# Optimization experiments

Measured on AMD Instinct MI355X. Metric: run time of the kernel, lower is better.

Reference implementation:

```python
import jax, jax.numpy as jnp
import numpy as np


def toeplitz_from(weight_matrix):
    # Faithful to the torch Toeplitz parametrization:
    # parameters = concat(W[::-1, 0], W[0, 1:]); toep[i, j] = parameters[n_rows-1-i+j]
    n_rows, n_cols = weight_matrix.shape
    params = jnp.concatenate([weight_matrix[::-1, 0], weight_matrix[0, 1:]])
    idx = (n_rows - 1) - jnp.arange(n_rows)[:, None] + jnp.arange(n_cols)[None, :]
    return params[idx]  # [n_rows, n_cols], built in one gather instead of a loop


def setup_inputs() -> dict:
    key = jax.random.key(0)
    ks = jax.random.split(key, 8)
    B, frame_dim, esn_dim, last_dim = 65536, 64, 960, 1024
    comb = frame_dim + esn_dim
    s1 = 1.0 / np.sqrt(comb)
    s2 = 1.0 / np.sqrt(last_dim)
    return {
        "x_frame": jax.random.normal(ks[0], (B, frame_dim), jnp.float32),
        "h_esn": jax.random.normal(ks[1], (B, esn_dim), jnp.float32),
        "W1": jax.random.normal(ks[2], (last_dim, comb), jnp.float32) * s1,
        "b1": jax.random.normal(ks[3], (last_dim,), jnp.float32) * s1,
        "W_slope": jax.random.normal(ks[4], (frame_dim, last_dim), jnp.float32) * s2,
        "b_slope": jax.random.normal(ks[5], (frame_dim,), jnp.float32) * s2,
        "W_int": jax.random.normal(ks[6], (frame_dim, last_dim), jnp.float32) * s2,
        "b_int": jax.random.normal(ks[7], (frame_dim,), jnp.float32) * s2,
    }


def reference(x_frame, h_esn, W1, b1, W_slope, b_slope, W_int, b_int):
    W1_toep = toeplitz_from(W1)                      # [last_dim, frame+esn]
    combined = jnp.concatenate([x_frame, h_esn], axis=-1)  # [B, frame+esn]
    q_last = jax.nn.relu(combined @ W1_toep.T + b1)  # [B, last_dim]
    slope = jnp.tanh(q_last @ W_slope.T + b_slope)   # [B, frame_dim]
    intercept = q_last @ W_int.T + b_int             # [B, frame_dim]
    return slope, intercept
```

## Files before the change

kernel.cpp:

```cpp
#include <hip/hip_runtime.h>
#include <cstdint>
#include <cstddef>

typedef __bf16 bf16x8v __attribute__((ext_vector_type(8)));
typedef float f32x4v __attribute__((ext_vector_type(4)));

__device__ __forceinline__ void gload_lds16(const void* g, void* l) {
  __builtin_amdgcn_global_load_lds((const __attribute__((address_space(1))) void*)g,
                                   (__attribute__((address_space(3))) void*)l,
                                   16, 0, 0);
}

__device__ __forceinline__ bf16x8v cvt_bf16x8(f32x4v a, f32x4v b) {
  bf16x8v r;
  r[0] = (__bf16)a[0]; r[1] = (__bf16)a[1]; r[2] = (__bf16)a[2]; r[3] = (__bf16)a[3];
  r[4] = (__bf16)b[0]; r[5] = (__bf16)b[1]; r[6] = (__bf16)b[2]; r[7] = (__bf16)b[3];
  return r;
}

__global__ __launch_bounds__(256) void prep_kernel(const float* __restrict__ W1,
                                                   const float* __restrict__ Wslope,
                                                   const float* __restrict__ Wint,
                                                   __bf16* __restrict__ toep,
                                                   __bf16* __restrict__ Wcat) {
  int id = blockIdx.x * 256 + threadIdx.x;
  if (id < 1024 * 1024) {
    int i = id >> 10, j = id & 1023;
    int p = 1023 - i + j;
    float v = (p < 1024) ? W1[(size_t)(1023 - p) << 10]
                         : W1[p - 1023];
    toep[id] = (__bf16)v;
  } else {
    int id2 = id - 1024 * 1024;
    int n = id2 >> 10, k = id2 & 1023;
    float v = (n < 64) ? Wslope[((size_t)n << 10) + k] : Wint[((size_t)(n - 64) << 10) + k];
    Wcat[id2] = (__bf16)v;
  }
}

__global__ __launch_bounds__(256) void gemm1_kernel(const float* __restrict__ x,
                                                    const float* __restrict__ h,
                                                    const __bf16* __restrict__ toep,
                                                    const float* __restrict__ b1,
                                                    __bf16* __restrict__ q) {
  __shared__ __align__(16) __bf16 At[128 * 32];
  __shared__ __align__(16) __bf16 Bt[128 * 32];
  const int tid = threadIdx.x;
  const int wid = tid >> 6;
  const int lane = tid & 63;
  const int wrow = wid >> 1, wcol = wid & 1;
  const int m0 = (blockIdx.x >> 3) << 7;
  const int n0 = (blockIdx.x & 7) << 7;
  const int quad = lane >> 4, l15 = lane & 15;
  const int rl = lane >> 2, seg = lane & 3;

  f32x4v acc[4][4] = {};

  auto a_ptr = [&](int k0, int t) -> const f32x4v* {
    const float* s; int ld, kk;
    if (k0 < 64) { s = x; ld = 64; kk = k0; } else { s = h; ld = 960; kk = k0 - 64; }
    int row = m0 + wid * 32 + t * 16 + rl;
    return (const f32x4v*)(s + (size_t)row * ld + kk + seg * 8);
  };

  f32x4v pv[2][2];
  {
    const f32x4v* p0 = a_ptr(0, 0); pv[0][0] = p0[0]; pv[0][1] = p0[1];
    const f32x4v* p1 = a_ptr(0, 1); pv[1][0] = p1[0]; pv[1][1] = p1[1];
  }

  for (int k0 = 0; k0 < 1024; k0 += 32) {
    __syncthreads();
    {
      int rb = wid * 32;
#pragma unroll
      for (int c = 0; c < 2; ++c) {
        int row = rb + c * 16 + rl;
        const __bf16* g = toep + (((size_t)(n0 + row)) << 10) + k0 + seg * 8;
        gload_lds16(g, &Bt[(rb + c * 16) * 32]);
      }
    }
#pragma unroll
    for (int t = 0; t < 2; ++t) {
      int row = wid * 32 + t * 16 + rl;
      *(bf16x8v*)&At[row * 32 + seg * 8] = cvt_bf16x8(pv[t][0], pv[t][1]);
    }
    __syncthreads();
    if (k0 + 32 < 1024) {
      const f32x4v* p0 = a_ptr(k0 + 32, 0);
      f32x4v n00 = p0[0], n01 = p0[1];
      const f32x4v* p1 = a_ptr(k0 + 32, 1);
      f32x4v n10 = p1[0], n11 = p1[1];
      pv[0][0] = n00; pv[0][1] = n01; pv[1][0] = n10; pv[1][1] = n11;
    }
    bf16x8v af[4], bfr[4];
#pragma unroll
    for (int r = 0; r < 4; ++r)
      af[r] = *(const bf16x8v*)&At[(wrow * 64 + r * 16 + l15) * 32 + quad * 8];
#pragma unroll
    for (int c = 0; c < 4; ++c)
      bfr[c] = *(const bf16x8v*)&Bt[(wcol * 64 + c * 16 + l15) * 32 + quad * 8];
#pragma unroll
    for (int r = 0; r < 4; ++r)
#pragma unroll
      for (int c = 0; c < 4; ++c)
        acc[r][c] = __builtin_amdgcn_mfma_f32_16x16x32_bf16(af[r], bfr[c], acc[r][c], 0, 0, 0);
  }

#pragma unroll
  for (int c = 0; c < 4; ++c) {
    int col = n0 + wcol * 64 + c * 16 + l15;
    float bias = b1[col];
#pragma unroll
    for (int r = 0; r < 4; ++r)
#pragma unroll
      for (int e = 0; e < 4; ++e) {
        int row = m0 + wrow * 64 + r * 16 + quad * 4 + e;
        float v = fmaxf(acc[r][c][e] + bias, 0.0f);
        q[((size_t)row << 10) + col] = (__bf16)v;
      }
  }
}

__global__ __launch_bounds__(256) void gemm2_kernel(const __bf16* __restrict__ q,
                                                    const __bf16* __restrict__ Wcat,
                                                    const float* __restrict__ b_slope,
                                                    const float* __restrict__ b_int,
                                                    float* __restrict__ out) {
  __shared__ __align__(16) __bf16 At[128 * 32];
  __shared__ __align__(16) __bf16 Bt[128 * 32];
  const int tid = threadIdx.x;
  const int wid = tid >> 6, lane = tid & 63;
  const int wrow = wid >> 1, wcol = wid & 1;
  const int m0 = blockIdx.x << 7;
  const int quad = lane >> 4, l15 = lane & 15;
  const int rl = lane >> 2, seg = lane & 3;

  f32x4v acc[4][4] = {};

  for (int k0 = 0; k0 < 1024; k0 += 32) {
    __syncthreads();
#pragma unroll
    for (int c = 0; c < 2; ++c) {
      int row = wid * 32 + c * 16 + rl;
      gload_lds16(q + (((size_t)(m0 + row)) << 10) + k0 + seg * 8, &At[(wid * 32 + c * 16) * 32]);
      gload_lds16(Wcat + (((size_t)row) << 10) + k0 + seg * 8, &Bt[(wid * 32 + c * 16) * 32]);
    }
    __syncthreads();
    bf16x8v af[4], bfr[4];
#pragma unroll
    for (int r = 0; r < 4; ++r)
      af[r] = *(const bf16x8v*)&At[(wrow * 64 + r * 16 + l15) * 32 + quad * 8];
#pragma unroll
    for (int c = 0; c < 4; ++c)
      bfr[c] = *(const bf16x8v*)&Bt[(wcol * 64 + c * 16 + l15) * 32 + quad * 8];
#pragma unroll
    for (int r = 0; r < 4; ++r)
#pragma unroll
      for (int c = 0; c < 4; ++c)
        acc[r][c] = __builtin_amdgcn_mfma_f32_16x16x32_bf16(af[r], bfr[c], acc[r][c], 0, 0, 0);
  }

#pragma unroll
  for (int c = 0; c < 4; ++c) {
    int col = wcol * 64 + c * 16 + l15;
    float bias = (col < 64) ? b_slope[col] : b_int[col - 64];
#pragma unroll
    for (int r = 0; r < 4; ++r)
#pragma unroll
      for (int e = 0; e < 4; ++e) {
        int row = m0 + wrow * 64 + r * 16 + quad * 4 + e;
        float v = acc[r][c][e] + bias;
        if (col < 64) {
          float xc = fminf(fmaxf(v, -15.f), 15.f);
          float t = __expf(2.f * xc);
          out[(size_t)row * 64 + col] = (t - 1.f) / (t + 1.f);
        } else {
          out[(size_t)4194304 + (size_t)row * 64 + (col - 64)] = v;
        }
      }
  }
}

extern "C" void kernel_launch(void* const* d_in, const int* in_sizes, int n_in,
                              void* d_out, int out_size, void* d_ws, size_t ws_size,
                              hipStream_t stream) {
  const float* x  = (const float*)d_in[0];
  const float* h  = (const float*)d_in[1];
  const float* W1 = (const float*)d_in[2];
  const float* b1 = (const float*)d_in[3];
  const float* Ws = (const float*)d_in[4];
  const float* bs = (const float*)d_in[5];
  const float* Wi = (const float*)d_in[6];
  const float* bi = (const float*)d_in[7];
  char* ws = (char*)d_ws;
  __bf16* q    = (__bf16*)ws;
  __bf16* toep = (__bf16*)(ws + (size_t)134217728);
  __bf16* Wcat = (__bf16*)(ws + (size_t)134217728 + (size_t)2097152);

  hipLaunchKernelGGL(prep_kernel,  dim3(4608), dim3(256), 0, stream, W1, Ws, Wi, toep, Wcat);
  hipLaunchKernelGGL(gemm1_kernel, dim3(4096), dim3(256), 0, stream, x, h, toep, b1, q);
  hipLaunchKernelGGL(gemm2_kernel, dim3(512),  dim3(256), 0, stream, q, Wcat, bs, bi, (float*)d_out);
}
```

Baseline: 648.7 us.

## Pre-pack inputs to bf16 and double-buffer both GEMMs with direct LDS loads

A separate pack kernel converts x/h into one concatenated bf16 activation matrix and builds the Toeplitz and output weights with vectorized writes from a small params vector. GEMM1 then loads both operands via global_load_lds into double-buffered LDS with one barrier per k-step, so register conversion and the second barrier leave the main loop. GEMM2 uses 64-row tiles with a k-step of 64 and double buffering, doubling its grid. The cost is an extra 128MB bf16 write and read of the activations plus a larger workspace, with a fallback to the old path when the workspace is too small.

```diff
diff --git a/kernel.cpp b/kernel.cpp
--- a/kernel.cpp
+++ b/kernel.cpp
@@ -16,6 +16,247 @@
   r[0] = (__bf16)a[0]; r[1] = (__bf16)a[1]; r[2] = (__bf16)a[2]; r[3] = (__bf16)a[3];
   r[4] = (__bf16)b[0]; r[5] = (__bf16)b[1]; r[6] = (__bf16)b[2]; r[7] = (__bf16)b[3];
   return r;
+}
+
+__global__ __launch_bounds__(256) void params_kernel(const float* __restrict__ W1,
+                                                     float* __restrict__ params) {
+  int p = blockIdx.x * 256 + threadIdx.x;
+  if (p < 2047)
+    params[p] = (p < 1024) ? W1[(size_t)(1023 - p) << 10] : W1[p - 1023];
+}
+
+__global__ __launch_bounds__(256) void pack_kernel(const float* __restrict__ x,
+                                                   const float* __restrict__ h,
+                                                   const float* __restrict__ params,
+                                                   const float* __restrict__ Ws,
+                                                   const float* __restrict__ Wi,
+                                                   __bf16* __restrict__ Acat,
+                                                   __bf16* __restrict__ toep,
+                                                   __bf16* __restrict__ Wcat) {
+  long u = (long)blockIdx.x * 256 + threadIdx.x;
+  if (u < 8388608L) {
+    int r = (int)(u >> 7), cg = (int)(u & 127);
+    const float* s = (cg < 8) ? x + (size_t)r * 64 + cg * 8
+                              : h + (size_t)r * 960 + (cg - 8) * 8;
+    f32x4v a = *(const f32x4v*)s, b = *(const f32x4v*)(s + 4);
+    *(bf16x8v*)(Acat + ((size_t)r << 10) + cg * 8) = cvt_bf16x8(a, b);
+  } else if (u < 8519680L) {
+    long t = u - 8388608L;
+    int i = (int)(t >> 7), j0 = (int)(t & 127) * 8;
+    const float* s = params + (1023 - i + j0);
+    bf16x8v o;
+#pragma unroll
+    for (int e = 0; e < 8; ++e) o[e] = (__bf16)s[e];
+    *(bf16x8v*)(toep + ((size_t)i << 10) + j0) = o;
+  } else {
+    long t = u - 8519680L;
+    int n = (int)(t >> 7), k0 = (int)(t & 127) * 8;
+    const float* s = (n < 64) ? Ws + ((size_t)n << 10) + k0
+                              : Wi + ((size_t)(n - 64) << 10) + k0;
+    f32x4v a = *(const f32x4v*)s, b = *(const f32x4v*)(s + 4);
+    *(bf16x8v*)(Wcat + ((size_t)n << 10) + k0) = cvt_bf16x8(a, b);
+  }
+}
+
+__global__ __launch_bounds__(256) void gemm1_dma(const __bf16* __restrict__ Acat,
+                                                 const __bf16* __restrict__ toep,
+                                                 const float* __restrict__ b1,
+                                                 __bf16* __restrict__ q) {
+  __shared__ __align__(16) __bf16 Ab[2][128 * 32];
+  __shared__ __align__(16) __bf16 Bb[2][128 * 32];
+  const int tid = threadIdx.x, wid = tid >> 6, lane = tid & 63;
+  const int wrow = wid >> 1, wcol = wid & 1;
+  const int m0 = (blockIdx.x >> 3) << 7;
+  const int n0 = (blockIdx.x & 7) << 7;
+  const int quad = lane >> 4, l15 = lane & 15;
+  const int rl = lane >> 2, seg = lane & 3;
+
+  f32x4v acc[4][4] = {};
+
+  auto stage = [&](int buf, int kt) {
+    int k0 = kt << 5;
+#pragma unroll
+    for (int c = 0; c < 2; ++c) {
+      int rb = wid * 32 + c * 16;
+      gload_lds16(Acat + (((size_t)(m0 + rb + rl)) << 10) + k0 + seg * 8, &Ab[buf][rb * 32]);
+      gload_lds16(toep + (((size_t)(n0 + rb + rl)) << 10) + k0 + seg * 8, &Bb[buf][rb * 32]);
+    }
+  };
+
+  stage(0, 0);
+  for (int kt = 0; kt < 32; ++kt) {
+    int cur = kt & 1;
+    __syncthreads();
+    if (kt < 31) stage(cur ^ 1, kt + 1);
+    bf16x8v af[4], bfr[4];
+#pragma unroll
+    for (int r = 0; r < 4; ++r)
+      af[r] = *(const bf16x8v*)&Ab[cur][(wrow * 64 + r * 16 + l15) * 32 + quad * 8];
+#pragma unroll
+    for (int c = 0; c < 4; ++c)
+      bfr[c] = *(const bf16x8v*)&Bb[cur][(wcol * 64 + c * 16 + l15) * 32 + quad * 8];
+#pragma unroll
+    for (int r = 0; r < 4; ++r)
+#pragma unroll
+      for (int c = 0; c < 4; ++c)
+        acc[r][c] = __builtin_amdgcn_mfma_f32_16x16x32_bf16(af[r], bfr[c], acc[r][c], 0, 0, 0);
+  }
+
+#pragma unroll
+  for (int c = 0; c < 4; ++c) {
+    int col = n0 + wcol * 64 + c * 16 + l15;
+    float bias = b1[col];
+#pragma unroll
+    for (int r = 0; r < 4; ++r)
+#pragma unroll
+      for (int e = 0; e < 4; ++e) {
+        int row = m0 + wrow * 64 + r * 16 + quad * 4 + e;
+        q[((size_t)row << 10) + col] = (__bf16)fmaxf(acc[r][c][e] + bias, 0.0f);
+      }
+  }
+}
+
+__global__ __launch_bounds__(256) void gemm1_fused(const float* __restrict__ x,
+                                                   const float* __restrict__ h,
+                                                   const __bf16* __restrict__ toep,
+                                                   const float* __restrict__ b1,
+                                                   __bf16* __restrict__ q) {
+  __shared__ __align__(16) __bf16 At[128 * 32];
+  __shared__ __align__(16) __bf16 Bt[128 * 32];
+  const int tid = threadIdx.x, wid = tid >> 6, lane = tid & 63;
+  const int wrow = wid >> 1, wcol = wid & 1;
+  const int m0 = (blockIdx.x >> 3) << 7;
+  const int n0 = (blockIdx.x & 7) << 7;
+  const int quad = lane >> 4, l15 = lane & 15;
+  const int rl = lane >> 2, seg = lane & 3;
+
+  f32x4v acc[4][4] = {};
+  auto a_ptr = [&](int k0, int t) -> const f32x4v* {
+    const float* s; int ld, kk;
+    if (k0 < 64) { s = x; ld = 64; kk = k0; } else { s = h; ld = 960; kk = k0 - 64; }
+    int row = m0 + wid * 32 + t * 16 + rl;
+    return (const f32x4v*)(s + (size_t)row * ld + kk + seg * 8);
+  };
+  f32x4v pv[2][2];
+  { const f32x4v* p0 = a_ptr(0, 0); pv[0][0] = p0[0]; pv[0][1] = p0[1];
+    const f32x4v* p1 = a_ptr(0, 1); pv[1][0] = p1[0]; pv[1][1] = p1[1]; }
+
+  for (int k0 = 0; k0 < 1024; k0 += 32) {
+    __syncthreads();
+    { int rb = wid * 32;
+#pragma unroll
+      for (int c = 0; c < 2; ++c) {
+        int row = rb + c * 16 + rl;
+        gload_lds16(toep + (((size_t)(n0 + row)) << 10) + k0 + seg * 8, &Bt[(rb + c * 16) * 32]);
+      } }
+#pragma unroll
+    for (int t = 0; t < 2; ++t) {
+      int row = wid * 32 + t * 16 + rl;
+      *(bf16x8v*)&At[row * 32 + seg * 8] = cvt_bf16x8(pv[t][0], pv[t][1]);
+    }
+    __syncthreads();
+    if (k0 + 32 < 1024) {
+      const f32x4v* p0 = a_ptr(k0 + 32, 0); f32x4v n00 = p0[0], n01 = p0[1];
+      const f32x4v* p1 = a_ptr(k0 + 32, 1); f32x4v n10 = p1[0], n11 = p1[1];
+      pv[0][0] = n00; pv[0][1] = n01; pv[1][0] = n10; pv[1][1] = n11;
+    }
+    bf16x8v af[4], bfr[4];
+#pragma unroll
+    for (int r = 0; r < 4; ++r)
+      af[r] = *(const bf16x8v*)&At[(wrow * 64 + r * 16 + l15) * 32 + quad * 8];
+#pragma unroll
+    for (int c = 0; c < 4; ++c)
+      bfr[c] = *(const bf16x8v*)&Bt[(wcol * 64 + c * 16 + l15) * 32 + quad * 8];
+#pragma unroll
+    for (int r = 0; r < 4; ++r)
+#pragma unroll
+      for (int c = 0; c < 4; ++c)
+        acc[r][c] = __builtin_amdgcn_mfma_f32_16x16x32_bf16(af[r], bfr[c], acc[r][c], 0, 0, 0);
+  }
+#pragma unroll
+  for (int c = 0; c < 4; ++c) {
+    int col = n0 + wcol * 64 + c * 16 + l15;
+    float bias = b1[col];
+#pragma unroll
+    for (int r = 0; r < 4; ++r)
+#pragma unroll
+      for (int e = 0; e < 4; ++e) {
+        int row = m0 + wrow * 64 + r * 16 + quad * 4 + e;
+        q[((size_t)row << 10) + col] = (__bf16)fmaxf(acc[r][c][e] + bias, 0.0f);
+      }
+  }
+}
+
+__global__ __launch_bounds__(256) void gemm2_dma(const __bf16* __restrict__ q,
+                                                 const __bf16* __restrict__ Wcat,
+                                                 const float* __restrict__ b_slope,
+                                                 const float* __restrict__ b_int,
+                                                 float* __restrict__ out) {
+  __shared__ __align__(16) __bf16 Ab[2][64 * 64];
+  __shared__ __align__(16) __bf16 Bb[2][128 * 64];
+  const int tid = threadIdx.x, wid = tid >> 6, lane = tid & 63;
+  const int wrow = wid >> 1, wcol = wid & 1;
+  const int m0 = blockIdx.x << 6;
+  const int quad = lane >> 4, l15 = lane & 15;
+  const int r8 = lane >> 3, s8 = lane & 7;
+
+  f32x4v acc[2][4] = {};
+
+  auto stage = [&](int buf, int kt) {
+    int k0 = kt << 6;
+#pragma unroll
+    for (int j = 0; j < 2; ++j) {
+      int rb = wid * 16 + j * 8;
+      gload_lds16(q + (((size_t)(m0 + rb + r8)) << 10) + k0 + s8 * 8, &Ab[buf][rb * 64]);
+    }
+#pragma unroll
+    for (int j = 0; j < 4; ++j) {
+      int rb = wid * 32 + j * 8;
+      gload_lds16(Wcat + (((size_t)(rb + r8)) << 10) + k0 + s8 * 8, &Bb[buf][rb * 64]);
+    }
+  };
+
+  stage(0, 0);
+  for (int kt = 0; kt < 16; ++kt) {
+    int cur = kt & 1;
+    __syncthreads();
+    if (kt < 15) stage(cur ^ 1, kt + 1);
+#pragma unroll
+    for (int s = 0; s < 2; ++s) {
+      bf16x8v af[2], bfr[4];
+#pragma unroll
+      for (int r = 0; r < 2; ++r)
+        af[r] = *(const bf16x8v*)&Ab[cur][(wrow * 32 + r * 16 + l15) * 64 + s * 32 + quad * 8];
+#pragma unroll
+      for (int c = 0; c < 4; ++c)
+        bfr[c] = *(const bf16x8v*)&Bb[cur][(wcol * 64 + c * 16 + l15) * 64 + s * 32 + quad * 8];
+#pragma unroll
+      for (int r = 0; r < 2; ++r)
+#pragma unroll
+        for (int c = 0; c < 4; ++c)
+          acc[r][c] = __builtin_amdgcn_mfma_f32_16x16x32_bf16(af[r], bfr[c], acc[r][c], 0, 0, 0);
+    }
+  }
+
+#pragma unroll
+  for (int c = 0; c < 4; ++c) {
+    int col = wcol * 64 + c * 16 + l15;
+    float bias = (col < 64) ? b_slope[col] : b_int[col - 64];
+#pragma unroll
+    for (int r = 0; r < 2; ++r)
+#pragma unroll
+      for (int e = 0; e < 4; ++e) {
+        int row = m0 + wrow * 32 + r * 16 + quad * 4 + e;
+        float v = acc[r][c][e] + bias;
+        if (col < 64) {
+          float xc = fminf(fmaxf(v, -15.f), 15.f);
+          float t = __expf(2.f * xc);
+          out[(size_t)row * 64 + col] = (t - 1.f) / (t + 1.f);
+        } else {
+          out[(size_t)4194304 + (size_t)row * 64 + (col - 64)] = v;
+        }
+      }
+  }
 }
 
 __global__ __launch_bounds__(256) void prep_kernel(const float* __restrict__ W1,
@@ -27,158 +268,13 @@
   if (id < 1024 * 1024) {
     int i = id >> 10, j = id & 1023;
     int p = 1023 - i + j;
-    float v = (p < 1024) ? W1[(size_t)(1023 - p) << 10]
-                         : W1[p - 1023];
+    float v = (p < 1024) ? W1[(size_t)(1023 - p) << 10] : W1[p - 1023];
     toep[id] = (__bf16)v;
   } else {
     int id2 = id - 1024 * 1024;
     int n = id2 >> 10, k = id2 & 1023;
     float v = (n < 64) ? Wslope[((size_t)n << 10) + k] : Wint[((size_t)(n - 64) << 10) + k];
     Wcat[id2] = (__bf16)v;
-  }
-}
-
-__global__ __launch_bounds__(256) void gemm1_kernel(const float* __restrict__ x,
-                                                    const float* __restrict__ h,
-                                                    const __bf16* __restrict__ toep,
-                                                    const float* __restrict__ b1,
-                                                    __bf16* __restrict__ q) {
-  __shared__ __align__(16) __bf16 At[128 * 32];
-  __shared__ __align__(16) __bf16 Bt[128 * 32];
-  const int tid = threadIdx.x;
-  const int wid = tid >> 6;
-  const int lane = tid & 63;
-  const int wrow = wid >> 1, wcol = wid & 1;
-  const int m0 = (blockIdx.x >> 3) << 7;
-  const int n0 = (blockIdx.x & 7) << 7;
-  const int quad = lane >> 4, l15 = lane & 15;
-  const int rl = lane >> 2, seg = lane & 3;
-
-  f32x4v acc[4][4] = {};
-
-  auto a_ptr = [&](int k0, int t) -> const f32x4v* {
-    const float* s; int ld, kk;
-    if (k0 < 64) { s = x; ld = 64; kk = k0; } else { s = h; ld = 960; kk = k0 - 64; }
-    int row = m0 + wid * 32 + t * 16 + rl;
-    return (const f32x4v*)(s + (size_t)row * ld + kk + seg * 8);
-  };
-
-  f32x4v pv[2][2];
-  {
-    const f32x4v* p0 = a_ptr(0, 0); pv[0][0] = p0[0]; pv[0][1] = p0[1];
-    const f32x4v* p1 = a_ptr(0, 1); pv[1][0] = p1[0]; pv[1][1] = p1[1];
-  }
-
-  for (int k0 = 0; k0 < 1024; k0 += 32) {
-    __syncthreads();
-    {
-      int rb = wid * 32;
-#pragma unroll
-      for (int c = 0; c < 2; ++c) {
-        int row = rb + c * 16 + rl;
-        const __bf16* g = toep + (((size_t)(n0 + row)) << 10) + k0 + seg * 8;
-        gload_lds16(g, &Bt[(rb + c * 16) * 32]);
-      }
-    }
-#pragma unroll
-    for (int t = 0; t < 2; ++t) {
-      int row = wid * 32 + t * 16 + rl;
-      *(bf16x8v*)&At[row * 32 + seg * 8] = cvt_bf16x8(pv[t][0], pv[t][1]);
-    }
-    __syncthreads();
-    if (k0 + 32 < 1024) {
-      const f32x4v* p0 = a_ptr(k0 + 32, 0);
-      f32x4v n00 = p0[0], n01 = p0[1];
-      const f32x4v* p1 = a_ptr(k0 + 32, 1);
-      f32x4v n10 = p1[0], n11 = p1[1];
-      pv[0][0] = n00; pv[0][1] = n01; pv[1][0] = n10; pv[1][1] = n11;
-    }
-    bf16x8v af[4], bfr[4];
-#pragma unroll
-    for (int r = 0; r < 4; ++r)
-      af[r] = *(const bf16x8v*)&At[(wrow * 64 + r * 16 + l15) * 32 + quad * 8];
-#pragma unroll
-    for (int c = 0; c < 4; ++c)
-      bfr[c] = *(const bf16x8v*)&Bt[(wcol * 64 + c * 16 + l15) * 32 + quad * 8];
-#pragma unroll
-    for (int r = 0; r < 4; ++r)
-#pragma unroll
-      for (int c = 0; c < 4; ++c)
-        acc[r][c] = __builtin_amdgcn_mfma_f32_16x16x32_bf16(af[r], bfr[c], acc[r][c], 0, 0, 0);
-  }
-
-#pragma unroll
-  for (int c = 0; c < 4; ++c) {
-    int col = n0 + wcol * 64 + c * 16 + l15;
-    float bias = b1[col];
-#pragma unroll
-    for (int r = 0; r < 4; ++r)
-#pragma unroll
-      for (int e = 0; e < 4; ++e) {
-        int row = m0 + wrow * 64 + r * 16 + quad * 4 + e;
-        float v = fmaxf(acc[r][c][e] + bias, 0.0f);
-        q[((size_t)row << 10) + col] = (__bf16)v;
-      }
-  }
-}
-
-__global__ __launch_bounds__(256) void gemm2_kernel(const __bf16* __restrict__ q,
-                                                    const __bf16* __restrict__ Wcat,
-                                                    const float* __restrict__ b_slope,
-                                                    const float* __restrict__ b_int,
-                                                    float* __restrict__ out) {
-  __shared__ __align__(16) __bf16 At[128 * 32];
-  __shared__ __align__(16) __bf16 Bt[128 * 32];
-  const int tid = threadIdx.x;
-  const int wid = tid >> 6, lane = tid & 63;
-  const int wrow = wid >> 1, wcol = wid & 1;
-  const int m0 = blockIdx.x << 7;
-  const int quad = lane >> 4, l15 = lane & 15;
-  const int rl = lane >> 2, seg = lane & 3;
-
-  f32x4v acc[4][4] = {};
-
-  for (int k0 = 0; k0 < 1024; k0 += 32) {
-    __syncthreads();
-#pragma unroll
-    for (int c = 0; c < 2; ++c) {
-      int row = wid * 32 + c * 16 + rl;
-      gload_lds16(q + (((size_t)(m0 + row)) << 10) + k0 + seg * 8, &At[(wid * 32 + c * 16) * 32]);
-      gload_lds16(Wcat + (((size_t)row) << 10) + k0 + seg * 8, &Bt[(wid * 32 + c * 16) * 32]);
-    }
-    __syncthreads();
-    bf16x8v af[4], bfr[4];
-#pragma unroll
-    for (int r = 0; r < 4; ++r)
-      af[r] = *(const bf16x8v*)&At[(wrow * 64 + r * 16 + l15) * 32 + quad * 8];
-#pragma unroll
-    for (int c = 0; c < 4; ++c)
-      bfr[c] = *(const bf16x8v*)&Bt[(wcol * 64 + c * 16 + l15) * 32 + quad * 8];
-#pragma unroll
-    for (int r = 0; r < 4; ++r)
-#pragma unroll
-      for (int c = 0; c < 4; ++c)
-        acc[r][c] = __builtin_amdgcn_mfma_f32_16x16x32_bf16(af[r], bfr[c], acc[r][c], 0, 0, 0);
-  }
-
-#pragma unroll
-  for (int c = 0; c < 4; ++c) {
-    int col = wcol * 64 + c * 16 + l15;
-    float bias = (col < 64) ? b_slope[col] : b_int[col - 64];
-#pragma unroll
-    for (int r = 0; r < 4; ++r)
-#pragma unroll
-      for (int e = 0; e < 4; ++e) {
-        int row = m0 + wrow * 64 + r * 16 + quad * 4 + e;
-        float v = acc[r][c][e] + bias;
-        if (col < 64) {
-          float xc = fminf(fmaxf(v, -15.f), 15.f);
-          float t = __expf(2.f * xc);
-          out[(size_t)row * 64 + col] = (t - 1.f) / (t + 1.f);
-        } else {
-          out[(size_t)4194304 + (size_t)row * 64 + (col - 64)] = v;
-        }
-      }
   }
 }
 
@@ -194,11 +290,31 @@
   const float* Wi = (const float*)d_in[6];
   const float* bi = (const float*)d_in[7];
   char* ws = (char*)d_ws;
-  __bf16* q    = (__bf16*)ws;
-  __bf16* toep = (__bf16*)(ws + (size_t)134217728);
-  __bf16* Wcat = (__bf16*)(ws + (size_t)134217728 + (size_t)2097152);
-
-  hipLaunchKernelGGL(prep_kernel,  dim3(4608), dim3(256), 0, stream, W1, Ws, Wi, toep, Wcat);
-  hipLaunchKernelGGL(gemm1_kernel, dim3(4096), dim3(256), 0, stream, x, h, toep, b1, q);
-  hipLaunchKernelGGL(gemm2_kernel, dim3(512),  dim3(256), 0, stream, q, Wcat, bs, bi, (float*)d_out);
-}
+
+  const size_t SZ_Q    = 134217728;
+  const size_t SZ_ACAT = 134217728;
+  const size_t SZ_TOEP = 2097152;
+  const size_t SZ_WCAT = 262144;
+  const size_t need = SZ_Q + SZ_ACAT + SZ_TOEP + SZ_WCAT + 8192;
+
+  __bf16* q = (__bf16*)ws;
+  if (ws_size >= need) {
+    __bf16* Acat  = (__bf16*)(ws + SZ_Q);
+    __bf16* toep  = (__bf16*)(ws + SZ_Q + SZ_ACAT);
+    __bf16* Wcat  = (__bf16*)(ws + SZ_Q + SZ_ACAT + SZ_TOEP);
+    float* params = (float*)(ws + SZ_Q + SZ_ACAT + SZ_TOEP + SZ_WCAT);
+    hipLaunchKernelGGL(params_kernel, dim3(8),     dim3(256), 0, stream, W1, params);
+    hipLaunchKernelGGL(pack_kernel,   dim3(33344), dim3(256), 0, stream,
+                       x, h, params, Ws, Wi, Acat, toep, Wcat);
+    hipLaunchKernelGGL(gemm1_dma,     dim3(4096),  dim3(256), 0, stream, Acat, toep, b1, q);
+    hipLaunchKernelGGL(gemm2_dma,     dim3(1024),  dim3(256), 0, stream, q, Wcat, bs, bi,
+                       (float*)d_out);
+  } else {
+    __bf16* toep = (__bf16*)(ws + SZ_Q);
+    __bf16* Wcat = (__bf16*)(ws + SZ_Q + SZ_TOEP);
+    hipLaunchKernelGGL(prep_kernel,   dim3(4608), dim3(256), 0, stream, W1, Ws, Wi, toep, Wcat);
+    hipLaunchKernelGGL(gemm1_fused,   dim3(4096), dim3(256), 0, stream, x, h, toep, b1, q);
+    hipLaunchKernelGGL(gemm2_dma,     dim3(1024), dim3(256), 0, stream, q, Wcat, bs, bi,
+                       (float*)d_out);
+  }
+}
```

Measured after the change: 659.6 us. No clear change (+1.7%).
